# Kernel optimization log

Measured on AMD Instinct MI355X. Metric: run time of the kernel, lower is better.

The kernel has to match this reference:

```python
import jax, jax.numpy as jnp
import numpy as np

NEG_SLOPE = 0.2  # PyG GATConv default negative_slope
N_NODES = 10000
N_EDGES = 320000
IN_CH = 512
HID = 128
HEADS = 4
N_CLASSES = 2


def gat_conv(x, src, dst, n, W, att_src, att_dst, bias, concat):
    """PyG-style GATConv (shared weights for src/dst, eval mode: no dropout)."""
    H, C = att_src.shape
    h = (x @ W).reshape(-1, H, C)                      # [N, H, C]
    a_src = jnp.sum(h * att_src[None], axis=-1)        # [N, H]
    a_dst = jnp.sum(h * att_dst[None], axis=-1)        # [N, H]
    e = a_src[src] + a_dst[dst]                        # [E, H]
    e = jnp.where(e > 0, e, NEG_SLOPE * e)             # LeakyReLU
    # numerically stable softmax over incoming edges of each dst node
    m = jax.ops.segment_max(e, dst, num_segments=n)    # [N, H]
    m = jnp.where(jnp.isfinite(m), m, 0.0)
    ex = jnp.exp(e - m[dst])
    denom = jax.ops.segment_sum(ex, dst, num_segments=n)
    alpha = ex / (denom[dst] + 1e-16)                  # [E, H]
    out = jax.ops.segment_sum(alpha[:, :, None] * h[src], dst, num_segments=n)  # [N,H,C]
    if concat:
        out = out.reshape(n, H * C)
    else:
        out = out.mean(axis=1)
    return out + bias


def setup_inputs() -> dict:
    key = jax.random.key(0)
    ks = jax.random.split(key, 8)
    x = jax.random.normal(ks[0], (N_NODES, IN_CH), dtype=jnp.float32)
    edge_index = jax.random.randint(ks[1], (2, N_EDGES), 0, N_NODES, dtype=jnp.int32)
    s1 = 1.0 / np.sqrt(IN_CH)
    s2 = 1.0 / np.sqrt(HEADS * HID)
    return {
        "x": x,
        "edge_index": edge_index,
        "W1": jax.random.normal(ks[2], (IN_CH, HEADS * HID), dtype=jnp.float32) * s1,
        "att_src1": jax.random.normal(ks[3], (HEADS, HID), dtype=jnp.float32) * s2,
        "att_dst1": jax.random.normal(ks[4], (HEADS, HID), dtype=jnp.float32) * s2,
        "b1": jnp.zeros((HEADS * HID,), dtype=jnp.float32),
        "W2": jax.random.normal(ks[5], (HEADS * HID, N_CLASSES), dtype=jnp.float32) * s2,
        "att_src2": jax.random.normal(ks[6], (1, N_CLASSES), dtype=jnp.float32),
        "att_dst2": jax.random.normal(ks[7], (1, N_CLASSES), dtype=jnp.float32),
        "b2": jnp.zeros((N_CLASSES,), dtype=jnp.float32),
    }


def reference(x, edge_index, W1, att_src1, att_dst1, b1, W2, att_src2, att_dst2, b2):
    n = x.shape[0]
    loop = jnp.arange(n, dtype=edge_index.dtype)       # PyG add_self_loops=True
    src = jnp.concatenate([edge_index[0], loop])
    dst = jnp.concatenate([edge_index[1], loop])
    h = gat_conv(x, src, dst, n, W1, att_src1, att_dst1, b1, concat=True)
    h = jax.nn.elu(h)
    out = gat_conv(h, src, dst, n, W2, att_src2, att_dst2, b2, concat=False)
    return out
```

## Files before the change

### kernel.cpp

```cpp
#include <hip/hip_runtime.h>
#include <hip/hip_bf16.h>

#define N_NODES 10000
#define N_EDGES 320000
#define E_TOT   330000
#define IN_CH   512
#define F1      512
#define HID     128
#define HEADS   4
#define SLOTS   128
#define MAXDEG  64

typedef __attribute__((ext_vector_type(8))) short bf16x8;
typedef __attribute__((ext_vector_type(4))) float f32x4;

__device__ __forceinline__ float lo16(unsigned u) { return __uint_as_float(u << 16); }
__device__ __forceinline__ float hi16(unsigned u) { return __uint_as_float(u & 0xffff0000u); }
__device__ __forceinline__ unsigned short bfbits(float f) {
    __hip_bfloat16 h = __float2bfloat16(f);
    return *(unsigned short*)&h;
}

__device__ __forceinline__ void gload_lds16(const void* g, void* l) {
    __builtin_amdgcn_global_load_lds(
        (const __attribute__((address_space(1))) unsigned int*)g,
        (__attribute__((address_space(3))) unsigned int*)l, 16, 0, 0);
}

__global__ void k_prep(const float* __restrict__ x, unsigned short* __restrict__ xb,
                       const float* __restrict__ w1, unsigned short* __restrict__ w1t,
                       int* __restrict__ zbase) {
    __shared__ float tile[64][65];
    int b = blockIdx.x;
    int t = threadIdx.x;
    if (b < 5000) {
        int idx = b * 256 + t;
        float4 v = ((const float4*)x)[idx];
        ushort4 u;
        u.x = bfbits(v.x); u.y = bfbits(v.y); u.z = bfbits(v.z); u.w = bfbits(v.w);
        ((ushort4*)xb)[idx] = u;
    } else if (b < 5064) {
        int bb = b - 5000;
        int bi = bb >> 3, bj = bb & 7;
        int r0 = t >> 6, col = t & 63;
#pragma unroll
        for (int p = 0; p < 16; ++p) {
            int row = p * 4 + r0;
            tile[row][col] = w1[(size_t)(bi * 64 + row) * 512 + bj * 64 + col];
        }
        __syncthreads();
#pragma unroll
        for (int p = 0; p < 16; ++p) {
            int row = p * 4 + r0;
            w1t[(size_t)(bj * 64 + row) * 512 + bi * 64 + col] = bfbits(tile[col][row]);
        }
    } else {
        int idx = (b - 5064) * 256 + t;
        if (idx < 130000) zbase[idx] = 0;
    }
}

#define GEMM_BLKS 316
__device__ __forceinline__ void gemm_step(const __hip_bfloat16* A, const __hip_bfloat16* B,
                                          int wr, int wc, int col16, int quad,
                                          f32x4 acc[4][4]) {
#pragma unroll
    for (int kk = 0; kk < 2; ++kk) {
        bf16x8 af[4], bf[4];
#pragma unroll
        for (int m = 0; m < 4; ++m) {
            int r = wr * 64 + m * 16 + col16;
            af[m] = *(const bf16x8*)((const char*)A + r * 128 +
                                     ((kk * 64 + quad * 16) ^ ((r & 7) << 4)));
        }
#pragma unroll
        for (int c = 0; c < 4; ++c) {
            int r = wc * 64 + c * 16 + col16;
            bf[c] = *(const bf16x8*)((const char*)B + r * 128 +
                                     ((kk * 64 + quad * 16) ^ ((r & 7) << 4)));
        }
#pragma unroll
        for (int m = 0; m < 4; ++m)
#pragma unroll
            for (int c = 0; c < 4; ++c)
                acc[m][c] = __builtin_amdgcn_mfma_f32_16x16x32_bf16(af[m], bf[c], acc[m][c], 0, 0, 0);
    }
}

__global__ __launch_bounds__(256) void k_gemm1(const __hip_bfloat16* __restrict__ xb,
                                               const __hip_bfloat16* __restrict__ w1t,
                                               const float* __restrict__ as_vec,
                                               const float* __restrict__ ad_vec,
                                               __hip_bfloat16* __restrict__ h1b,
                                               float* __restrict__ a_src,
                                               float* __restrict__ a_dst,
                                               const int* __restrict__ src,
                                               const int* __restrict__ dst,
                                               int* __restrict__ cnt,
                                               int* __restrict__ slots) {
    if (blockIdx.x >= GEMM_BLKS) {
        int e = (blockIdx.x - GEMM_BLKS) * 256 + threadIdx.x;
        if (e < E_TOT) {
            int d, s;
            if (e < N_EDGES) { d = dst[e]; s = src[e]; } else { d = e - N_EDGES; s = d; }
            int pos = atomicAdd(&cnt[d], 1);
            if (pos < SLOTS) slots[d * SLOTS + pos] = s;
        }
        return;
    }
    __shared__ __align__(16) __hip_bfloat16 lsA[2][128 * 64];
    __shared__ __align__(16) __hip_bfloat16 lsB[2][128 * 64];
    int nt = blockIdx.x & 3;
    int mt = blockIdx.x >> 2;
    int row0 = mt * 128;
    int t = threadIdx.x;
    int lane = t & 63;
    int wid = t >> 6;
    int wr = wid >> 1, wc = wid & 1;
    int col16 = lane & 15, quad = lane >> 4;

    const __hip_bfloat16* ga[4];
    const __hip_bfloat16* gb[4];
    unsigned loff[4];
#pragma unroll
    for (int p = 0; p < 4; ++p) {
        int ci = p * 256 + t;
        int row = ci >> 3, ch = ci & 7;
        int sch = ch ^ (row & 7);
        ga[p] = xb + (size_t)min(row0 + row, N_NODES - 1) * IN_CH + sch * 8;
        gb[p] = w1t + (size_t)(nt * 128 + row) * IN_CH + sch * 8;
        loff[p] = ci * 16;
    }

    f32x4 acc[4][4] = {};

#pragma unroll
    for (int p = 0; p < 4; ++p) gload_lds16(ga[p], (char*)lsA[0] + loff[p]);
#pragma unroll
    for (int p = 0; p < 4; ++p) gload_lds16(gb[p], (char*)lsB[0] + loff[p]);
    __syncthreads();

#pragma unroll 1
    for (int s = 0; s < 7; ++s) {
        int nb = (s + 1) & 1, kt = (s + 1) * 64;
#pragma unroll
        for (int p = 0; p < 4; ++p) gload_lds16(ga[p] + kt, (char*)lsA[nb] + loff[p]);
#pragma unroll
        for (int p = 0; p < 4; ++p) gload_lds16(gb[p] + kt, (char*)lsB[nb] + loff[p]);
        gemm_step(lsA[s & 1], lsB[s & 1], wr, wc, col16, quad, acc);
        __syncthreads();
    }
    gemm_step(lsA[1], lsB[1], wr, wc, col16, quad, acc);

    float asv[4], adv[4];
#pragma unroll
    for (int c = 0; c < 4; ++c) {
        int col = nt * 128 + wc * 64 + c * 16 + col16;
        asv[c] = as_vec[col];
        adv[c] = ad_vec[col];
    }
#pragma unroll
    for (int m = 0; m < 4; ++m) {
#pragma unroll
        for (int reg = 0; reg < 4; ++reg) {
            int row = row0 + wr * 64 + m * 16 + quad * 4 + reg;
            bool ok = row < N_NODES;
            float ps = 0.f, pd = 0.f;
#pragma unroll
            for (int c = 0; c < 4; ++c) {
                float v = acc[m][c][reg];
                ps += v * asv[c];
                pd += v * adv[c];
                if (ok) h1b[(size_t)row * F1 + nt * 128 + wc * 64 + c * 16 + col16] =
                            __float2bfloat16(v);
            }
#pragma unroll
            for (int off = 1; off <= 8; off <<= 1) {
                ps += __shfl_xor(ps, off);
                pd += __shfl_xor(pd, off);
            }
            if (col16 == 0 && ok) {
                atomicAdd(&a_src[nt * N_NODES + row], ps);
                atomicAdd(&a_dst[nt * N_NODES + row], pd);
            }
        }
    }
}

#define CONSUME(D, W)                                                   \
    do {                                                                \
        float ww_ = (W);                                                \
        acc[0] += ww_ * lo16((D).x); acc[1] += ww_ * hi16((D).x);       \
        acc[2] += ww_ * lo16((D).y); acc[3] += ww_ * hi16((D).y);       \
        acc[4] += ww_ * lo16((D).z); acc[5] += ww_ * hi16((D).z);       \
        acc[6] += ww_ * lo16((D).w); acc[7] += ww_ * hi16((D).w);       \
    } while (0)

__global__ __launch_bounds__(256, 4) void k_aggr1(const __hip_bfloat16* __restrict__ h1b,
                                               const float* __restrict__ a_src,
                                               const float* __restrict__ a_dst,
                                               const int* __restrict__ cnt,
                                               const int* __restrict__ slots,
                                               const float* __restrict__ b1,
                                               const float* __restrict__ w2,
                                               const float* __restrict__ as2,
                                               const float* __restrict__ ad2,
                                               float* __restrict__ h2,
                                               float* __restrict__ a_src2,
                                               float* __restrict__ a_dst2) {
    __shared__ int2 wlds[4][MAXDEG];
    int h = blockIdx.x & 3;
    int w = threadIdx.x >> 6;
    int n = (blockIdx.x >> 2) * 4 + w;
    int lane = threadIdx.x & 63;
    const int* sl = slots + n * SLOTS;

    int s_raw = sl[lane];
    int cn = min(cnt[n], MAXDEG);
    float adst = a_dst[h * N_NODES + n];
    bool live = lane < cn;
    int s = live ? s_raw : 0;
    float e = a_src[h * N_NODES + s] + adst;
    e = fmaxf(e, 0.2f * e);
    float wgt = live ? __expf(e) : 0.f;
    float dsum = wgt;
#pragma unroll
    for (int off = 1; off < 64; off <<= 1) dsum += __shfl_xor(dsum, off);
    int2 pw; pw.x = s << 10;
    pw.y = __float_as_int(wgt);
    wlds[w][lane] = pw;

    int q = lane >> 4, c16 = lane & 15;
    const char* hb = (const char*)h1b + h * 256 + c16 * 16;
    float acc[8] = {};
    int kmax = (cn + 3) >> 2;
    int np = (kmax + 1) >> 1;
    int i1 = min(1, np - 1);
    int2 pA0 = wlds[w][q],            pA1 = wlds[w][4 + q];
    uint4 dA0 = *(const uint4*)(hb + pA0.x);
    uint4 dA1 = *(const uint4*)(hb + pA1.x);
    int2 pB0 = wlds[w][i1 * 8 + q],   pB1 = wlds[w][i1 * 8 + 4 + q];
    uint4 dB0 = *(const uint4*)(hb + pB0.x);
    uint4 dB1 = *(const uint4*)(hb + pB1.x);
#pragma unroll 1
    for (int i = 0; i < np; i += 2) {
        CONSUME(dA0, __int_as_float(pA0.y));
        CONSUME(dA1, __int_as_float(pA1.y));
        int nxa = i + 2;
        if (nxa < np) {
            pA0 = wlds[w][nxa * 8 + q]; pA1 = wlds[w][nxa * 8 + 4 + q];
            dA0 = *(const uint4*)(hb + pA0.x);
            dA1 = *(const uint4*)(hb + pA1.x);
        }
        if (i + 1 < np) {
            CONSUME(dB0, __int_as_float(pB0.y));
            CONSUME(dB1, __int_as_float(pB1.y));
            int nxb = i + 3;
            if (nxb < np) {
                pB0 = wlds[w][nxb * 8 + q]; pB1 = wlds[w][nxb * 8 + 4 + q];
                dB0 = *(const uint4*)(hb + pB0.x);
                dB1 = *(const uint4*)(hb + pB1.x);
            }
        }
    }
#pragma unroll
    for (int j = 0; j < 8; ++j) {
        acc[j] += __shfl_xor(acc[j], 16);
        acc[j] += __shfl_xor(acc[j], 32);
    }
    float inv = 1.f / (dsum + 1e-16f);
    int c0 = h * 128 + c16 * 8;
    float ps0 = 0.f, ps1 = 0.f;
#pragma unroll
    for (int j = 0; j < 8; ++j) {
        float v = acc[j] * inv + b1[c0 + j];
        v = v > 0.f ? v : __expf(v) - 1.f;
        ps0 += v * w2[(c0 + j) * 2 + 0];
        ps1 += v * w2[(c0 + j) * 2 + 1];
    }
#pragma unroll
    for (int off = 1; off <= 8; off <<= 1) {
        ps0 += __shfl_xor(ps0, off);
        ps1 += __shfl_xor(ps1, off);
    }
    if (lane == 0) {
        atomicAdd(&h2[n * 2 + 0], ps0);
        atomicAdd(&h2[n * 2 + 1], ps1);
        atomicAdd(&a_src2[n], ps0 * as2[0] + ps1 * as2[1]);
        atomicAdd(&a_dst2[n], ps0 * ad2[0] + ps1 * ad2[1]);
    }
}

__global__ __launch_bounds__(256) void k_aggr2(const float* __restrict__ h2,
                                               const float* __restrict__ a_src2,
                                               const float* __restrict__ a_dst2,
                                               const int* __restrict__ cnt,
                                               const int* __restrict__ slots,
                                               const float* __restrict__ b2,
                                               float* __restrict__ out) {
    int lane = threadIdx.x & 63;
    int sub = lane >> 4, slot = lane & 15;
    int n = blockIdx.x * 16 + (threadIdx.x >> 6) * 4 + sub;
    int cn = min(cnt[n], SLOTS);
    const int* sl = slots + n * SLOTS;
    float adst = a_dst2[n];
    float dsum = 0.f, acc0 = 0.f, acc1 = 0.f;
    for (int i = slot; i < cn; i += 16) {
        int s = sl[i];
        float e = a_src2[s] + adst;
        e = fmaxf(e, 0.2f * e);
        float w = __expf(e);
        dsum += w;
        acc0 += w * h2[s * 2 + 0];
        acc1 += w * h2[s * 2 + 1];
    }
#pragma unroll
    for (int off = 1; off <= 8; off <<= 1) {
        dsum += __shfl_xor(dsum, off);
        acc0 += __shfl_xor(acc0, off);
        acc1 += __shfl_xor(acc1, off);
    }
    if (slot == 0) {
        float inv = 1.f / (dsum + 1e-16f);
        out[n * 2 + 0] = acc0 * inv + b2[0];
        out[n * 2 + 1] = acc1 * inv + b2[1];
    }
}

extern "C" void kernel_launch(void* const* d_in, const int* in_sizes, int n_in,
                              void* d_out, int out_size, void* d_ws, size_t ws_size,
                              hipStream_t stream) {
    const float* x   = (const float*)d_in[0];
    const int*   ei  = (const int*)d_in[1];
    const float* W1  = (const float*)d_in[2];
    const float* as1 = (const float*)d_in[3];
    const float* ad1 = (const float*)d_in[4];
    const float* b1  = (const float*)d_in[5];
    const float* W2  = (const float*)d_in[6];
    const float* as2 = (const float*)d_in[7];
    const float* ad2 = (const float*)d_in[8];
    const float* b2  = (const float*)d_in[9];

    char* ws = (char*)d_ws;
    __hip_bfloat16* h1b = (__hip_bfloat16*)(ws);
    __hip_bfloat16* xb  = (__hip_bfloat16*)(ws + 10240000);
    __hip_bfloat16* w1t = (__hip_bfloat16*)(ws + 20480000);
    const size_t S = 21004288;
    float* a_src1 = (float*)(ws + S);
    float* a_dst1 = (float*)(ws + S + 160000);
    float* h2     = (float*)(ws + S + 320000);
    float* a_src2 = (float*)(ws + S + 400000);
    float* a_dst2 = (float*)(ws + S + 440000);
    int*   cnt    = (int*)(ws + S + 480000);
    int*   slots  = (int*)(ws + S + 520000);

    const int* srcArr = ei;
    const int* dstArr = ei + N_EDGES;

    k_prep<<<5064 + 508, 256, 0, stream>>>(x, (unsigned short*)xb, W1,
                                           (unsigned short*)w1t, (int*)a_src1);
    k_gemm1<<<GEMM_BLKS + 1290, 256, 0, stream>>>(xb, w1t, as1, ad1, h1b,
                                                  a_src1, a_dst1,
                                                  srcArr, dstArr, cnt, slots);
    k_aggr1<<<N_NODES, 256, 0, stream>>>(h1b, a_src1, a_dst1, cnt, slots, b1,
                                         W2, as2, ad2, h2, a_src2, a_dst2);
    k_aggr2<<<N_NODES / 16, 256, 0, stream>>>(h2, a_src2, a_dst2, cnt, slots, b2,
                                              (float*)d_out);
}
```

Before: 157.5 us.

## Pipeline edge-feature gathers through an 8-deep LDS ring with async global-to-LDS loads

Replaces the register double-buffered gather of neighbour features in the layer-1 aggregation with an 8-stage ring of direct global-to-LDS loads per wave, gated by vmcnt waits. This keeps more gathers in flight to hide random-access latency. It adds 32KB of LDS per block, which may lower occupancy under the 4-blocks launch bound, and the waits rely on exact vmcnt accounting.

```diff
diff --git a/kernel.cpp b/kernel.cpp
--- a/kernel.cpp
+++ b/kernel.cpp
@@ -209,6 +209,7 @@
                                                float* __restrict__ a_src2,
                                                float* __restrict__ a_dst2) {
     __shared__ int2 wlds[4][MAXDEG];
+    __shared__ __align__(16) char ring[4][8][1024];
     int h = blockIdx.x & 3;
     int w = threadIdx.x >> 6;
     int n = (blockIdx.x >> 2) * 4 + w;
@@ -231,37 +232,37 @@
     wlds[w][lane] = pw;
 
     int q = lane >> 4, c16 = lane & 15;
-    const char* hb = (const char*)h1b + h * 256 + c16 * 16;
+    const char* hbase = (const char*)h1b + h * 256 + c16 * 16;
+    char* myring = &ring[w][0][0];
+    int G = (cn + 3) >> 2;
     float acc[8] = {};
-    int kmax = (cn + 3) >> 2;
-    int np = (kmax + 1) >> 1;
-    int i1 = min(1, np - 1);
-    int2 pA0 = wlds[w][q],            pA1 = wlds[w][4 + q];
-    uint4 dA0 = *(const uint4*)(hb + pA0.x);
-    uint4 dA1 = *(const uint4*)(hb + pA1.x);
-    int2 pB0 = wlds[w][i1 * 8 + q],   pB1 = wlds[w][i1 * 8 + 4 + q];
-    uint4 dB0 = *(const uint4*)(hb + pB0.x);
-    uint4 dB1 = *(const uint4*)(hb + pB1.x);
+
+    int issued = min(G, 8);
 #pragma unroll 1
-    for (int i = 0; i < np; i += 2) {
-        CONSUME(dA0, __int_as_float(pA0.y));
-        CONSUME(dA1, __int_as_float(pA1.y));
-        int nxa = i + 2;
-        if (nxa < np) {
-            pA0 = wlds[w][nxa * 8 + q]; pA1 = wlds[w][nxa * 8 + 4 + q];
-            dA0 = *(const uint4*)(hb + pA0.x);
-            dA1 = *(const uint4*)(hb + pA1.x);
-        }
-        if (i + 1 < np) {
-            CONSUME(dB0, __int_as_float(pB0.y));
-            CONSUME(dB1, __int_as_float(pB1.y));
-            int nxb = i + 3;
-            if (nxb < np) {
-                pB0 = wlds[w][nxb * 8 + q]; pB1 = wlds[w][nxb * 8 + 4 + q];
-                dB0 = *(const uint4*)(hb + pB0.x);
-                dB1 = *(const uint4*)(hb + pB1.x);
-            }
-        }
+    for (int g = 0; g < issued; ++g) {
+        int2 pe = wlds[w][g * 4 + q];
+        gload_lds16(hbase + pe.x, myring + (size_t)(g & 7) * 1024 + lane * 16);
+    }
+    int steady = G - 8;
+#pragma unroll 1
+    for (int g = 0; g < steady; ++g) {
+        __builtin_amdgcn_sched_barrier(0);
+        asm volatile("s_waitcnt vmcnt(7)" ::: "memory");
+        __builtin_amdgcn_sched_barrier(0);
+        int2 pe = wlds[w][g * 4 + q];
+        uint4 d = *(const uint4*)(myring + (size_t)(g & 7) * 1024 + lane * 16);
+        CONSUME(d, __int_as_float(pe.y));
+        int2 pn = wlds[w][(g + 8) * 4 + q];
+        gload_lds16(hbase + pn.x, myring + (size_t)(g & 7) * 1024 + lane * 16);
+    }
+    __builtin_amdgcn_sched_barrier(0);
+    asm volatile("s_waitcnt vmcnt(0)" ::: "memory");
+    __builtin_amdgcn_sched_barrier(0);
+#pragma unroll 1
+    for (int g = (steady > 0 ? steady : 0); g < G; ++g) {
+        int2 pe = wlds[w][g * 4 + q];
+        uint4 d = *(const uint4*)(myring + (size_t)(g & 7) * 1024 + lane * 16);
+        CONSUME(d, __int_as_float(pe.y));
     }
 #pragma unroll
     for (int j = 0; j < 8; ++j) {
```

Measured after the change: 169.2 us. 1.07x slower.
